# Performance work log

Measured on AMD Instinct MI355X. Metric: run time of the kernel, lower is better.

## Reference

```python
import jax, jax.numpy as jnp
import numpy as np

D_EMB = 1024
D_ATTN = 1024
NUM_HEADS = 16
HEAD_DIM = D_ATTN // NUM_HEADS
SEQ = 2048
BS = 2


def setup_inputs() -> dict:
    key = jax.random.key(0)
    ks = jax.random.split(key, 6)
    s = 1.0 / np.sqrt(D_EMB)
    return {
        "x": jax.random.normal(ks[0], (BS, SEQ, D_EMB), dtype=jnp.float32),
        "W_q": jax.random.uniform(ks[1], (D_ATTN, D_EMB), jnp.float32, -s, s),
        "W_k": jax.random.uniform(ks[2], (D_ATTN, D_EMB), jnp.float32, -s, s),
        "W_v": jax.random.uniform(ks[3], (D_ATTN, D_EMB), jnp.float32, -s, s),
        "W_o": jax.random.uniform(ks[4], (D_ATTN, D_ATTN), jnp.float32, -s, s),
        "b_o": jax.random.uniform(ks[5], (D_ATTN,), jnp.float32, -s, s),
    }


def reference(x, W_q, W_k, W_v, W_o, b_o):
    bs, seq_len, _ = x.shape
    # QKV projections (torch Linear: x @ W.T)
    q = jnp.einsum('bse,ae->bsa', x, W_q).reshape(bs, seq_len, NUM_HEADS, HEAD_DIM)
    k = jnp.einsum('bse,ae->bsa', x, W_k).reshape(bs, seq_len, NUM_HEADS, HEAD_DIM)
    v = jnp.einsum('bse,ae->bsa', x, W_v).reshape(bs, seq_len, NUM_HEADS, HEAD_DIM)
    # [b, h, s, d]
    q = q.transpose(0, 2, 1, 3)
    k = k.transpose(0, 2, 1, 3)
    v = v.transpose(0, 2, 1, 3)
    # scores [b, h, s, s] with causal mask
    scores = jnp.einsum('bhqd,bhkd->bhqk', q, k)
    causal = jnp.tril(jnp.ones((seq_len, seq_len), dtype=bool))
    scores = jnp.where(causal, scores, -jnp.inf)
    attn = jax.nn.softmax(scores / np.sqrt(HEAD_DIM), axis=-1)
    # dropout p=0.0 -> identity
    ctx = jnp.einsum('bhqk,bhkd->bhqd', attn, v)
    ctx = ctx.transpose(0, 2, 1, 3).reshape(bs, seq_len, D_ATTN)
    return jnp.einsum('bsa,oa->bso', ctx, W_o) + b_o
```

## Files before the change

kernel.cpp:

```cpp
#include <hip/hip_runtime.h>
#include <stdint.h>

#define SEQ   2048
#define DEMB  1024
#define NH    16
#define HD    64
#define MROWS 4096

typedef __bf16 bf16x8 __attribute__((ext_vector_type(8)));
typedef __bf16 bf16x4 __attribute__((ext_vector_type(4)));
typedef float  f32x4  __attribute__((ext_vector_type(4)));

#define MFMA(a, b, c) __builtin_amdgcn_mfma_f32_16x16x32_bf16((a), (b), (c), 0, 0, 0)

static __device__ __forceinline__ uint16_t f2bf(float f) {
  union { __bf16 b; uint16_t u; } c;
  c.b = (__bf16)f;
  return c.u;
}

static __device__ __forceinline__ ushort4 pack4(f32x4 f) {
  union { bf16x4 b; ushort4 u; } c;
  c.b[0] = (__bf16)f[0]; c.b[1] = (__bf16)f[1];
  c.b[2] = (__bf16)f[2]; c.b[3] = (__bf16)f[3];
  return c.u;
}

static __device__ __forceinline__ bf16x8 ldb8(const uint16_t* p) {
  union { uint4 i; bf16x8 b; } u;
  u.i = *(const uint4*)p;
  return u.b;
}

static __device__ __forceinline__ void gld_lds16(const uint16_t* g, uint16_t* l) {
  __builtin_amdgcn_global_load_lds(
      (const __attribute__((address_space(1))) uint32_t*)(g),
      (__attribute__((address_space(3))) uint32_t*)(l),
      16, 0, 0);
}

__global__ __launch_bounds__(256) void cvt_all(const float* __restrict__ x,
                                               const float* __restrict__ wq,
                                               const float* __restrict__ wk,
                                               const float* __restrict__ wv,
                                               const float* __restrict__ wo,
                                               uint16_t* __restrict__ xb,
                                               uint16_t* __restrict__ wqkv,
                                               uint16_t* __restrict__ wob) {
  const int bid = blockIdx.x;
  const float* src; uint16_t* dst; int off;
  if (bid < 4096)      { src = x;  dst = xb;                 off = bid; }
  else if (bid < 5120) { src = wq; dst = wqkv;               off = bid - 4096; }
  else if (bid < 6144) { src = wk; dst = wqkv + (1u << 20);  off = bid - 5120; }
  else if (bid < 7168) { src = wv; dst = wqkv + (2u << 20);  off = bid - 6144; }
  else                 { src = wo; dst = wob;                off = bid - 7168; }
  const int i = (off * 256 + threadIdx.x) * 4;
  float4 v = *(const float4*)(src + i);
  f32x4 f; f[0] = v.x; f[1] = v.y; f[2] = v.z; f[3] = v.w;
  *(ushort4*)(dst + i) = pack4(f);
}

__global__ __launch_bounds__(512, 2) void gemm_qkv(const uint16_t* __restrict__ A,
                                                   const uint16_t* __restrict__ B,
                                                   uint16_t* __restrict__ Cq,
                                                   uint16_t* __restrict__ Ck,
                                                   uint16_t* __restrict__ Cvt) {
  constexpr int K = 1024;
  __shared__ uint16_t lds[57344];

  const int bcol = blockIdx.x * 192;
  const int brow = blockIdx.y << 8;

  const int t  = threadIdx.x;
  const int l  = t & 63;
  const int li = l & 15, lg = l >> 4;
  const int w  = t >> 6;
  const int wm = w >> 2;
  const int wn = w & 3;

  const int srow = t >> 3;
  const int scol = ((t & 7) ^ (srow & 7)) << 3;
  const uint16_t* gA = A + (size_t)(brow + srow) * K + scol;
  const uint16_t* gB = B + (size_t)(bcol + srow) * K + scol;

  auto stage = [&](int buf, int k0) {
    uint16_t* as = lds + buf * 16384;
    uint16_t* bs = lds + 32768 + buf * 12288;
    gld_lds16(gA + k0,                    as + t * 8);
    gld_lds16(gA + (size_t)64 * K + k0,   as + 4096 + t * 8);
    gld_lds16(gA + (size_t)128 * K + k0,  as + 8192 + t * 8);
    gld_lds16(gA + (size_t)192 * K + k0,  as + 12288 + t * 8);
    gld_lds16(gB + k0,                    bs + t * 8);
    gld_lds16(gB + (size_t)64 * K + k0,   bs + 4096 + t * 8);
    gld_lds16(gB + (size_t)128 * K + k0,  bs + 8192 + t * 8);
  };

  const int sw = li & 7;
  auto ldA = [&](int buf, int kh, int fi) {
    const int row = wm * 128 + fi * 16 + li;
    return ldb8(&lds[buf * 16384 + (row << 6) + ((((kh << 2) + lg) ^ sw) << 3)]);
  };
  auto ldB = [&](int buf, int kh, int ni) {
    const int row = wn * 48 + ni * 16 + li;
    return ldb8(&lds[32768 + buf * 12288 + (row << 6) + ((((kh << 2) + lg) ^ sw) << 3)]);
  };

  f32x4 acc[8][3] = {};

  stage(0, 0);
  __syncthreads();
  int cur = 0;

  for (int k0 = 0; k0 < K; k0 += 64) {
    if (k0 + 64 < K) stage(cur ^ 1, k0 + 64);

#pragma unroll
    for (int kh = 0; kh < 2; ++kh) {
      bf16x8 af[8], bfr[3];
#pragma unroll
      for (int ni = 0; ni < 3; ++ni) bfr[ni] = ldB(cur, kh, ni);
#pragma unroll
      for (int fi = 0; fi < 8; ++fi) af[fi] = ldA(cur, kh, fi);
      __builtin_amdgcn_s_setprio(1);
#pragma unroll
      for (int fi = 0; fi < 8; ++fi)
#pragma unroll
        for (int ni = 0; ni < 3; ++ni)
          acc[fi][ni] = MFMA(af[fi], bfr[ni], acc[fi][ni]);
      __builtin_amdgcn_s_setprio(0);
    }

    __syncthreads();
    cur ^= 1;
  }

  uint16_t* slab = lds + w * 6800;
  bool anyV = false;

#pragma unroll
  for (int mi = 0; mi < 8; ++mi) {
#pragma unroll
    for (int ni = 0; ni < 3; ++ni) {
      const int col = bcol + wn * 48 + ni * 16 + li;
      const int row = brow + wm * 128 + mi * 16 + lg * 4;
      if (col < 1024) {
#pragma unroll
        for (int r = 0; r < 4; ++r)
          Cq[(size_t)(row + r) * 1024 + col] = f2bf(acc[mi][ni][r] * 0.18033688f);
      } else if (col < 2048) {
#pragma unroll
        for (int r = 0; r < 4; ++r)
          Ck[(size_t)(row + r) * 1024 + (col - 1024)] = f2bf(acc[mi][ni][r]);
      } else {
        anyV = true;
        *(ushort4*)&slab[(ni * 16 + li) * 136 + mi * 16 + lg * 4] = pack4(acc[mi][ni]);
      }
    }
  }

  if (anyV) {
    asm volatile("s_waitcnt lgkmcnt(0)" ::: "memory");
    const int m0 = brow + wm * 128;
    const size_t mbase = (size_t)((m0 >> 11) << 10) * 2048 + (m0 & 2047);
#pragma unroll
    for (int cc = 0; cc < 12; ++cc) {
      const int c_loc = cc * 4 + lg;
      const int cglob = bcol + wn * 48 + c_loc;
      if (cglob >= 2048) {
        const int c = cglob - 2048;
        uint4 v = *(const uint4*)&slab[c_loc * 136 + li * 8];
        *(uint4*)(Cvt + (size_t)c * 2048 + mbase + li * 8) = v;
      }
    }
  }
}

__global__ __launch_bounds__(512, 2) void gemm_out(const uint16_t* __restrict__ A,
                                                   const uint16_t* __restrict__ B,
                                                   float* __restrict__ Cf,
                                                   const float* __restrict__ bias) {
  constexpr int K = 1024;
  __shared__ uint16_t As[2][128 * 64];
  __shared__ uint16_t Bs[2][128 * 64];

  const int bcol = blockIdx.x << 7;
  const int brow = blockIdx.y << 7;

  const int t  = threadIdx.x;
  const int l  = t & 63;
  const int li = l & 15, lg = l >> 4;
  const int w  = t >> 6;
  const int wm = w >> 2;
  const int wn = w & 3;

  const int srow = t >> 3;
  const int scol = ((t & 7) ^ (srow & 7)) << 3;
  const uint16_t* gA = A + (size_t)(brow + srow) * K + scol;
  const uint16_t* gB = B + (size_t)(bcol + srow) * K + scol;

  auto stage = [&](int buf, int k0) {
    gld_lds16(gA + k0,                  &As[buf][t * 8]);
    gld_lds16(gA + (size_t)64 * K + k0, &As[buf][4096 + t * 8]);
    gld_lds16(gB + k0,                  &Bs[buf][t * 8]);
    gld_lds16(gB + (size_t)64 * K + k0, &Bs[buf][4096 + t * 8]);
  };

  const int sw = li & 7;
  auto ldA = [&](int buf, int kh, int fi) {
    const int row = wm * 64 + fi * 16 + li;
    return ldb8(&As[buf][(row << 6) + ((((kh << 2) + lg) ^ sw) << 3)]);
  };
  auto ldB = [&](int buf, int kh, int ni) {
    const int row = wn * 32 + ni * 16 + li;
    return ldb8(&Bs[buf][(row << 6) + ((((kh << 2) + lg) ^ sw) << 3)]);
  };

  f32x4 acc[4][2] = {};

  stage(0, 0);
  __syncthreads();
  int cur = 0;

  for (int k0 = 0; k0 < K; k0 += 64) {
    if (k0 + 64 < K) stage(cur ^ 1, k0 + 64);

#pragma unroll
    for (int kh = 0; kh < 2; ++kh) {
      bf16x8 af[4], bfr[2];
#pragma unroll
      for (int ni = 0; ni < 2; ++ni) bfr[ni] = ldB(cur, kh, ni);
#pragma unroll
      for (int fi = 0; fi < 4; ++fi) af[fi] = ldA(cur, kh, fi);
      __builtin_amdgcn_s_setprio(1);
#pragma unroll
      for (int fi = 0; fi < 4; ++fi)
#pragma unroll
        for (int ni = 0; ni < 2; ++ni)
          acc[fi][ni] = MFMA(af[fi], bfr[ni], acc[fi][ni]);
      __builtin_amdgcn_s_setprio(0);
    }

    __syncthreads();
    cur ^= 1;
  }

#pragma unroll
  for (int mi = 0; mi < 4; ++mi) {
#pragma unroll
    for (int ni = 0; ni < 2; ++ni) {
      const int row = brow + wm * 64 + mi * 16 + lg * 4;
      const int col = bcol + wn * 32 + ni * 16 + li;
      const float bv = bias[col];
#pragma unroll
      for (int r = 0; r < 4; ++r)
        Cf[(size_t)(row + r) * 1024 + col] = acc[mi][ni][r] + bv;
    }
  }
}

__global__ __launch_bounds__(256, 3) void attn_fwd(const uint16_t* __restrict__ Q,
                                                   const uint16_t* __restrict__ K,
                                                   const uint16_t* __restrict__ Vt,
                                                   uint16_t* __restrict__ ctx) {
  const int id   = blockIdx.x;
  const int rank = id >> 3;
  const int bh   = (id & 7) * 4 + (rank >> 4);
  const int pr   = rank & 15;
  const int b = bh >> 4, h = bh & 15;

  const int t  = threadIdx.x;
  const int w  = t >> 6, l = t & 63;
  const int li = l & 15, lg = l >> 4;

  __shared__ uint16_t Kl[2][64 * 64];
  __shared__ uint16_t Vl[2][64 * 64];
  __shared__ uint16_t P[4][16][72];

  const uint16_t* Kg = K + (size_t)(b * 2048) * 1024 + h * 64;
  const uint16_t* Vg = Vt + (size_t)(b * 1024 + h * 64) * 2048;

  const int srow = t >> 3;
  const int scol = ((t & 7) * 8) ^ ((srow & 7) * 8);

  auto stage = [&](int buf, int kt2) {
    const int kb2 = kt2 << 6;
    gld_lds16(Kg + (size_t)(kb2 + srow) * 1024 + scol,      &Kl[buf][t * 8]);
    gld_lds16(Kg + (size_t)(kb2 + 32 + srow) * 1024 + scol, &Kl[buf][2048 + t * 8]);
    gld_lds16(Vg + (size_t)srow * 2048 + kb2 + scol,        &Vl[buf][t * 8]);
    gld_lds16(Vg + (size_t)(32 + srow) * 2048 + kb2 + scol, &Vl[buf][2048 + t * 8]);
  };

  const int fsw = (li & 7) * 8;
  int cur = 0;

#pragma unroll 1
  for (int ph = 0; ph < 2; ++ph) {
    const int qbl  = ph ? (31 - pr) : pr;
    const int qrow = (qbl << 6) + (w << 4);
    const uint16_t* qp = Q + (size_t)(b * 2048 + qrow + li) * 1024 + h * 64 + lg * 8;
    const bf16x8 q0 = ldb8(qp);
    const bf16x8 q1 = ldb8(qp + 32);

    f32x4 o[4] = {};
    float l_r = 0.f;

    stage(cur, 0);
    __syncthreads();

    for (int kt = 0; kt <= qbl; ++kt) {
      if (kt < qbl) stage(cur ^ 1, kt + 1);

      const uint16_t* Kc = &Kl[cur][0];
      const uint16_t* Vc = &Vl[cur][0];

      f32x4 s[4];
      __builtin_amdgcn_s_setprio(1);
#pragma unroll
      for (int tt = 0; tt < 4; ++tt) {
        const uint16_t* kr = Kc + (tt * 16 + li) * 64;
        f32x4 z = {};
        z = MFMA(ldb8(kr + ((lg * 8) ^ fsw)), q0, z);
        z = MFMA(ldb8(kr + ((32 + lg * 8) ^ fsw)), q1, z);
        s[tt] = z;
      }
      __builtin_amdgcn_s_setprio(0);

      bf16x8 vf[4][2];
#pragma unroll
      for (int dt = 0; dt < 4; ++dt) {
        const uint16_t* vr = Vc + (dt * 16 + li) * 64;
        vf[dt][0] = ldb8(vr + ((lg * 8) ^ fsw));
        vf[dt][1] = ldb8(vr + ((32 + lg * 8) ^ fsw));
      }

      if (kt == qbl) {
        const int qloc = (w << 4) + li;
#pragma unroll
        for (int tt = 0; tt < 4; ++tt) {
          const int key = (tt << 4) + (lg << 2);
#pragma unroll
          for (int r = 0; r < 4; ++r)
            if (key + r > qloc) s[tt][r] = -1e30f;
        }
      }

      float lsum = 0.f;
      ushort4 pk[4];
#pragma unroll
      for (int tt = 0; tt < 4; ++tt) {
        f32x4 p;
        p[0] = __builtin_amdgcn_exp2f(s[tt][0]);
        p[1] = __builtin_amdgcn_exp2f(s[tt][1]);
        p[2] = __builtin_amdgcn_exp2f(s[tt][2]);
        p[3] = __builtin_amdgcn_exp2f(s[tt][3]);
        lsum += (p[0] + p[1]) + (p[2] + p[3]);
        pk[tt] = pack4(p);
      }
      l_r += lsum;

#pragma unroll
      for (int tt = 0; tt < 4; ++tt)
        *(ushort4*)&P[w][li][(tt << 4) + (lg << 2)] = pk[tt];
      asm volatile("s_waitcnt lgkmcnt(0)" ::: "memory");

      const bf16x8 pb0 = ldb8(&P[w][li][lg * 8]);
      const bf16x8 pb1 = ldb8(&P[w][li][32 + lg * 8]);
      __builtin_amdgcn_s_setprio(1);
#pragma unroll
      for (int dt = 0; dt < 4; ++dt) {
        o[dt] = MFMA(vf[dt][0], pb0, o[dt]);
        o[dt] = MFMA(vf[dt][1], pb1, o[dt]);
      }
      __builtin_amdgcn_s_setprio(0);

      __syncthreads();
      cur ^= 1;
    }

    l_r += __shfl_xor(l_r, 16);
    l_r += __shfl_xor(l_r, 32);
    const float inv = 1.0f / l_r;
    const int qg = b * 2048 + qrow + li;
#pragma unroll
    for (int dt = 0; dt < 4; ++dt) {
      f32x4 ov = o[dt];
      ov[0] *= inv; ov[1] *= inv; ov[2] *= inv; ov[3] *= inv;
      *(ushort4*)(ctx + (size_t)qg * 1024 + h * 64 + (dt << 4) + (lg << 2)) = pack4(ov);
    }
  }
}

extern "C" void kernel_launch(void* const* d_in, const int* in_sizes, int n_in,
                              void* d_out, int out_size, void* d_ws, size_t ws_size,
                              hipStream_t stream) {
  const float* x  = (const float*)d_in[0];
  const float* Wq = (const float*)d_in[1];
  const float* Wk = (const float*)d_in[2];
  const float* Wv = (const float*)d_in[3];
  const float* Wo = (const float*)d_in[4];
  const float* bo = (const float*)d_in[5];
  float* out = (float*)d_out;

  char* ws = (char*)d_ws;
  uint16_t* xb   = (uint16_t*)(ws);
  uint16_t* Wqkv = (uint16_t*)(ws + ( 8u << 20));
  uint16_t* Wob  = (uint16_t*)(ws + (14u << 20));
  uint16_t* Qb   = (uint16_t*)(ws + (16u << 20));
  uint16_t* Kb   = (uint16_t*)(ws + (24u << 20));
  uint16_t* Vt   = (uint16_t*)(ws + (32u << 20));
  uint16_t* Ctx  = (uint16_t*)(ws);

  cvt_all<<<8192, 256, 0, stream>>>(x, Wq, Wk, Wv, Wo, xb, Wqkv, Wob);

  gemm_qkv<<<dim3(16, 16), 512, 0, stream>>>(xb, Wqkv, Qb, Kb, Vt);

  attn_fwd<<<512, 256, 0, stream>>>(Qb, Kb, Vt, Ctx);

  gemm_out<<<dim3(8, 32), 512, 0, stream>>>(Ctx, Wob, out, bo);
}
```

Baseline: 99.12 us.

## Triple-buffer LDS prefetch with vmcnt-gated barriers in GEMMs and attention

Replaces double buffering with a deeper prefetch pipeline in all three hot kernels. The QKV GEMM keeps three A buffers and two B buffers, while the output GEMM and the attention kernel keep three buffers, loading two tiles ahead. Each iteration waits with explicit s_waitcnt vmcnt plus a raw barrier instead of __syncthreads, so later loads stay in flight while the current tile is computed. The aim is to hide global-to-LDS latency. The cost is much larger LDS use, which likely lowers blocks per CU for the GEMMs. The attention launch bound is also lowered from 3 to 2.

Measured after the change: 100.7 us. About the same (+1.6%).

```diff
diff --git a/kernel.cpp b/kernel.cpp
--- a/kernel.cpp
+++ b/kernel.cpp
@@ -12,6 +12,7 @@
 typedef float  f32x4  __attribute__((ext_vector_type(4)));
 
 #define MFMA(a, b, c) __builtin_amdgcn_mfma_f32_16x16x32_bf16((a), (b), (c), 0, 0, 0)
+#define VMCNT(n) asm volatile("s_waitcnt vmcnt(" #n ")" ::: "memory")
 
 static __device__ __forceinline__ uint16_t f2bf(float f) {
   union { __bf16 b; uint16_t u; } c;
@@ -66,7 +67,7 @@
                                                    uint16_t* __restrict__ Ck,
                                                    uint16_t* __restrict__ Cvt) {
   constexpr int K = 1024;
-  __shared__ uint16_t lds[57344];
+  __shared__ uint16_t lds[73728];
 
   const int bcol = blockIdx.x * 192;
   const int brow = blockIdx.y << 8;
@@ -83,13 +84,15 @@
   const uint16_t* gA = A + (size_t)(brow + srow) * K + scol;
   const uint16_t* gB = B + (size_t)(bcol + srow) * K + scol;
 
-  auto stage = [&](int buf, int k0) {
+  auto stageA = [&](int buf, int k0) {
     uint16_t* as = lds + buf * 16384;
-    uint16_t* bs = lds + 32768 + buf * 12288;
     gld_lds16(gA + k0,                    as + t * 8);
     gld_lds16(gA + (size_t)64 * K + k0,   as + 4096 + t * 8);
     gld_lds16(gA + (size_t)128 * K + k0,  as + 8192 + t * 8);
     gld_lds16(gA + (size_t)192 * K + k0,  as + 12288 + t * 8);
+  };
+  auto stageB = [&](int buf, int k0) {
+    uint16_t* bs = lds + 49152 + buf * 12288;
     gld_lds16(gB + k0,                    bs + t * 8);
     gld_lds16(gB + (size_t)64 * K + k0,   bs + 4096 + t * 8);
     gld_lds16(gB + (size_t)128 * K + k0,  bs + 8192 + t * 8);
@@ -102,25 +105,30 @@
   };
   auto ldB = [&](int buf, int kh, int ni) {
     const int row = wn * 48 + ni * 16 + li;
-    return ldb8(&lds[32768 + buf * 12288 + (row << 6) + ((((kh << 2) + lg) ^ sw) << 3)]);
+    return ldb8(&lds[49152 + buf * 12288 + (row << 6) + ((((kh << 2) + lg) ^ sw) << 3)]);
   };
 
   f32x4 acc[8][3] = {};
 
-  stage(0, 0);
-  __syncthreads();
-  int cur = 0;
-
-  for (int k0 = 0; k0 < K; k0 += 64) {
-    if (k0 + 64 < K) stage(cur ^ 1, k0 + 64);
-
+  stageB(0, 0);
+  stageA(0, 0);
+  stageA(1, 64);
+  VMCNT(4);
+  __builtin_amdgcn_s_barrier();
+
+  for (int kt = 0; kt < 16; ++kt) {
+    const int k0 = kt << 6;
+    if (kt + 1 < 16) stageB((kt + 1) & 1, k0 + 64);
+    if (kt + 2 < 16) stageA((kt + 2) % 3, k0 + 128);
+
+    const int ab = kt % 3, bb = kt & 1;
 #pragma unroll
     for (int kh = 0; kh < 2; ++kh) {
       bf16x8 af[8], bfr[3];
 #pragma unroll
-      for (int ni = 0; ni < 3; ++ni) bfr[ni] = ldB(cur, kh, ni);
-#pragma unroll
-      for (int fi = 0; fi < 8; ++fi) af[fi] = ldA(cur, kh, fi);
+      for (int ni = 0; ni < 3; ++ni) bfr[ni] = ldB(bb, kh, ni);
+#pragma unroll
+      for (int fi = 0; fi < 8; ++fi) af[fi] = ldA(ab, kh, fi);
       __builtin_amdgcn_s_setprio(1);
 #pragma unroll
       for (int fi = 0; fi < 8; ++fi)
@@ -130,9 +138,14 @@
       __builtin_amdgcn_s_setprio(0);
     }
 
-    __syncthreads();
-    cur ^= 1;
-  }
+    if (kt + 1 < 16) {
+      if (kt + 2 < 16) VMCNT(4);
+      else             VMCNT(0);
+      __builtin_amdgcn_s_barrier();
+    }
+  }
+
+  __syncthreads();
 
   uint16_t* slab = lds + w * 6800;
   bool anyV = false;
@@ -180,8 +193,7 @@
                                                    float* __restrict__ Cf,
                                                    const float* __restrict__ bias) {
   constexpr int K = 1024;
-  __shared__ uint16_t As[2][128 * 64];
-  __shared__ uint16_t Bs[2][128 * 64];
+  __shared__ uint16_t lds[49152];
 
   const int bcol = blockIdx.x << 7;
   const int brow = blockIdx.y << 7;
@@ -199,38 +211,43 @@
   const uint16_t* gB = B + (size_t)(bcol + srow) * K + scol;
 
   auto stage = [&](int buf, int k0) {
-    gld_lds16(gA + k0,                  &As[buf][t * 8]);
-    gld_lds16(gA + (size_t)64 * K + k0, &As[buf][4096 + t * 8]);
-    gld_lds16(gB + k0,                  &Bs[buf][t * 8]);
-    gld_lds16(gB + (size_t)64 * K + k0, &Bs[buf][4096 + t * 8]);
+    uint16_t* as = lds + buf * 8192;
+    uint16_t* bs = lds + 24576 + buf * 8192;
+    gld_lds16(gA + k0,                  as + t * 8);
+    gld_lds16(gA + (size_t)64 * K + k0, as + 4096 + t * 8);
+    gld_lds16(gB + k0,                  bs + t * 8);
+    gld_lds16(gB + (size_t)64 * K + k0, bs + 4096 + t * 8);
   };
 
   const int sw = li & 7;
   auto ldA = [&](int buf, int kh, int fi) {
     const int row = wm * 64 + fi * 16 + li;
-    return ldb8(&As[buf][(row << 6) + ((((kh << 2) + lg) ^ sw) << 3)]);
+    return ldb8(&lds[buf * 8192 + (row << 6) + ((((kh << 2) + lg) ^ sw) << 3)]);
   };
   auto ldB = [&](int buf, int kh, int ni) {
     const int row = wn * 32 + ni * 16 + li;
-    return ldb8(&Bs[buf][(row << 6) + ((((kh << 2) + lg) ^ sw) << 3)]);
+    return ldb8(&lds[24576 + buf * 8192 + (row << 6) + ((((kh << 2) + lg) ^ sw) << 3)]);
   };
 
   f32x4 acc[4][2] = {};
 
   stage(0, 0);
-  __syncthreads();
-  int cur = 0;
-
-  for (int k0 = 0; k0 < K; k0 += 64) {
-    if (k0 + 64 < K) stage(cur ^ 1, k0 + 64);
-
+  stage(1, 64);
+  VMCNT(4);
+  __builtin_amdgcn_s_barrier();
+
+  for (int kt = 0; kt < 16; ++kt) {
+    const int k0 = kt << 6;
+    if (kt + 2 < 16) stage((kt + 2) % 3, k0 + 128);
+
+    const int cb = kt % 3;
 #pragma unroll
     for (int kh = 0; kh < 2; ++kh) {
       bf16x8 af[4], bfr[2];
 #pragma unroll
-      for (int ni = 0; ni < 2; ++ni) bfr[ni] = ldB(cur, kh, ni);
-#pragma unroll
-      for (int fi = 0; fi < 4; ++fi) af[fi] = ldA(cur, kh, fi);
+      for (int ni = 0; ni < 2; ++ni) bfr[ni] = ldB(cb, kh, ni);
+#pragma unroll
+      for (int fi = 0; fi < 4; ++fi) af[fi] = ldA(cb, kh, fi);
       __builtin_amdgcn_s_setprio(1);
 #pragma unroll
       for (int fi = 0; fi < 4; ++fi)
@@ -240,8 +257,11 @@
       __builtin_amdgcn_s_setprio(0);
     }
 
-    __syncthreads();
-    cur ^= 1;
+    if (kt + 1 < 16) {
+      if (kt + 2 < 16) VMCNT(4);
+      else             VMCNT(0);
+      __builtin_amdgcn_s_barrier();
+    }
   }
 
 #pragma unroll
@@ -258,7 +278,7 @@
   }
 }
 
-__global__ __launch_bounds__(256, 3) void attn_fwd(const uint16_t* __restrict__ Q,
+__global__ __launch_bounds__(256, 2) void attn_fwd(const uint16_t* __restrict__ Q,
                                                    const uint16_t* __restrict__ K,
                                                    const uint16_t* __restrict__ Vt,
                                                    uint16_t* __restrict__ ctx) {
@@ -272,8 +292,8 @@
   const int w  = t >> 6, l = t & 63;
   const int li = l & 15, lg = l >> 4;
 
-  __shared__ uint16_t Kl[2][64 * 64];
-  __shared__ uint16_t Vl[2][64 * 64];
+  __shared__ uint16_t Kl[3][64 * 64];
+  __shared__ uint16_t Vl[3][64 * 64];
   __shared__ uint16_t P[4][16][72];
 
   const uint16_t* Kg = K + (size_t)(b * 2048) * 1024 + h * 64;
@@ -291,11 +311,11 @@
   };
 
   const int fsw = (li & 7) * 8;
-  int cur = 0;
 
 #pragma unroll 1
   for (int ph = 0; ph < 2; ++ph) {
     const int qbl  = ph ? (31 - pr) : pr;
+    const int nkt  = qbl + 1;
     const int qrow = (qbl << 6) + (w << 4);
     const uint16_t* qp = Q + (size_t)(b * 2048 + qrow + li) * 1024 + h * 64 + lg * 8;
     const bf16x8 q0 = ldb8(qp);
@@ -304,14 +324,16 @@
     f32x4 o[4] = {};
     float l_r = 0.f;
 
-    stage(cur, 0);
-    __syncthreads();
-
-    for (int kt = 0; kt <= qbl; ++kt) {
-      if (kt < qbl) stage(cur ^ 1, kt + 1);
-
-      const uint16_t* Kc = &Kl[cur][0];
-      const uint16_t* Vc = &Vl[cur][0];
+    stage(0, 0);
+    stage(1, 1);
+    VMCNT(4);
+    __builtin_amdgcn_s_barrier();
+
+    for (int kt = 0; kt < nkt; ++kt) {
+      if (kt + 2 < nkt) stage((kt + 2) % 3, kt + 2);
+
+      const uint16_t* Kc = &Kl[kt % 3][0];
+      const uint16_t* Vc = &Vl[kt % 3][0];
 
       f32x4 s[4];
       __builtin_amdgcn_s_setprio(1);
@@ -373,9 +395,14 @@
       }
       __builtin_amdgcn_s_setprio(0);
 
-      __syncthreads();
-      cur ^= 1;
-    }
+      if (kt + 1 < nkt) {
+        if (kt + 2 < nkt) VMCNT(4);
+        else              VMCNT(0);
+        __builtin_amdgcn_s_barrier();
+      }
+    }
+
+    __syncthreads();
 
     l_r += __shfl_xor(l_r, 16);
     l_r += __shfl_xor(l_r, 32);
```

## Widen attention key tile to 128 with split K/V waits and reuse K buffer for P

Applied to the files above, without the earlier changes.

The attention kernel now processes 128 keys per iteration instead of 64, halving loop trips and barriers per query block. K and V are staged into separate LDS regions with explicit vmcnt waits, so QK^T can start once K has landed while V is still loading. The P scratch is carved out of the current K buffer after a barrier, removing the separate P array. LDS use doubles and occupancy drops from 3 to 2 blocks per SM. The diagonal tile now does extra masked work because of the coarser tile granularity.

Result: no change. 97.67 us (median of 2 runs) (-1.5%).

```diff
diff --git a/kernel.cpp b/kernel.cpp
--- a/kernel.cpp
+++ b/kernel.cpp
@@ -12,6 +12,13 @@
 typedef float  f32x4  __attribute__((ext_vector_type(4)));
 
 #define MFMA(a, b, c) __builtin_amdgcn_mfma_f32_16x16x32_bf16((a), (b), (c), 0, 0, 0)
+#define VMCNT(n) asm volatile("s_waitcnt vmcnt(" #n ")" ::: "memory")
+
+static __device__ __forceinline__ void bar() {
+  asm volatile("" ::: "memory");
+  __builtin_amdgcn_s_barrier();
+  asm volatile("" ::: "memory");
+}
 
 static __device__ __forceinline__ uint16_t f2bf(float f) {
   union { __bf16 b; uint16_t u; } c;
@@ -258,7 +265,7 @@
   }
 }
 
-__global__ __launch_bounds__(256, 3) void attn_fwd(const uint16_t* __restrict__ Q,
+__global__ __launch_bounds__(256, 2) void attn_fwd(const uint16_t* __restrict__ Q,
                                                    const uint16_t* __restrict__ K,
                                                    const uint16_t* __restrict__ Vt,
                                                    uint16_t* __restrict__ ctx) {
@@ -272,108 +279,113 @@
   const int w  = t >> 6, l = t & 63;
   const int li = l & 15, lg = l >> 4;
 
-  __shared__ uint16_t Kl[2][64 * 64];
-  __shared__ uint16_t Vl[2][64 * 64];
-  __shared__ uint16_t P[4][16][72];
+  __shared__ uint16_t Kl[2][128 * 64];
+  __shared__ uint16_t Vl[2][64 * 128];
 
   const uint16_t* Kg = K + (size_t)(b * 2048) * 1024 + h * 64;
   const uint16_t* Vg = Vt + (size_t)(b * 1024 + h * 64) * 2048;
 
-  const int srow = t >> 3;
-  const int scol = ((t & 7) * 8) ^ ((srow & 7) * 8);
-
-  auto stage = [&](int buf, int kt2) {
-    const int kb2 = kt2 << 6;
-    gld_lds16(Kg + (size_t)(kb2 + srow) * 1024 + scol,      &Kl[buf][t * 8]);
-    gld_lds16(Kg + (size_t)(kb2 + 32 + srow) * 1024 + scol, &Kl[buf][2048 + t * 8]);
-    gld_lds16(Vg + (size_t)srow * 2048 + kb2 + scol,        &Vl[buf][t * 8]);
-    gld_lds16(Vg + (size_t)(32 + srow) * 2048 + kb2 + scol, &Vl[buf][2048 + t * 8]);
-  };
-
-  const int fsw = (li & 7) * 8;
-  int cur = 0;
+  const int krow  = t >> 3;
+  const int kscol = ((t & 7) ^ (krow & 7)) << 3;
+  const int vrow  = t >> 4;
+  const int vscol = ((t & 15) ^ vrow) << 3;
+
+  auto stageK = [&](int buf, int kb) {
+#pragma unroll
+    for (int c = 0; c < 4; ++c)
+      gld_lds16(Kg + (size_t)(kb + c * 32 + krow) * 1024 + kscol,
+                &Kl[buf][c * 2048 + t * 8]);
+  };
+  auto stageV = [&](int buf, int kb) {
+#pragma unroll
+    for (int c = 0; c < 4; ++c)
+      gld_lds16(Vg + (size_t)(c * 16 + vrow) * 2048 + kb + vscol,
+                &Vl[buf][c * 2048 + t * 8]);
+  };
+
+  const int fsw = li & 7;
 
 #pragma unroll 1
   for (int ph = 0; ph < 2; ++ph) {
-    const int qbl  = ph ? (31 - pr) : pr;
+    const int qbl = ph ? (31 - pr) : pr;
+    const int nkt = (qbl >> 1) + 1;
     const int qrow = (qbl << 6) + (w << 4);
+    const int qglob = qrow + li;
     const uint16_t* qp = Q + (size_t)(b * 2048 + qrow + li) * 1024 + h * 64 + lg * 8;
-    const bf16x8 q0 = ldb8(qp);
-    const bf16x8 q1 = ldb8(qp + 32);
+    const bf16x8 q0v = ldb8(qp);
+    const bf16x8 q1v = ldb8(qp + 32);
 
     f32x4 o[4] = {};
     float l_r = 0.f;
-
-    stage(cur, 0);
-    __syncthreads();
-
-    for (int kt = 0; kt <= qbl; ++kt) {
-      if (kt < qbl) stage(cur ^ 1, kt + 1);
-
-      const uint16_t* Kc = &Kl[cur][0];
-      const uint16_t* Vc = &Vl[cur][0];
-
-      f32x4 s[4];
+    int cur = 0;
+
+    stageK(0, 0);
+    stageV(0, 0);
+    VMCNT(4);
+    bar();
+
+    for (int kt = 0; kt < nkt; ++kt) {
+      const int kb = kt << 7;
+      const bool pf = (kt + 1 < nkt);
+      if (pf) { stageK(cur ^ 1, kb + 128); stageV(cur ^ 1, kb + 128); }
+
+      f32x4 s[8];
       __builtin_amdgcn_s_setprio(1);
 #pragma unroll
-      for (int tt = 0; tt < 4; ++tt) {
-        const uint16_t* kr = Kc + (tt * 16 + li) * 64;
+      for (int tt = 0; tt < 8; ++tt) {
+        const uint16_t* kr = &Kl[cur][(tt * 16 + li) << 6];
         f32x4 z = {};
-        z = MFMA(ldb8(kr + ((lg * 8) ^ fsw)), q0, z);
-        z = MFMA(ldb8(kr + ((32 + lg * 8) ^ fsw)), q1, z);
+        z = MFMA(ldb8(kr + ((lg ^ fsw) << 3)), q0v, z);
+        z = MFMA(ldb8(kr + (((4 + lg) ^ fsw) << 3)), q1v, z);
         s[tt] = z;
       }
       __builtin_amdgcn_s_setprio(0);
 
-      bf16x8 vf[4][2];
-#pragma unroll
-      for (int dt = 0; dt < 4; ++dt) {
-        const uint16_t* vr = Vc + (dt * 16 + li) * 64;
-        vf[dt][0] = ldb8(vr + ((lg * 8) ^ fsw));
-        vf[dt][1] = ldb8(vr + ((32 + lg * 8) ^ fsw));
-      }
-
-      if (kt == qbl) {
-        const int qloc = (w << 4) + li;
-#pragma unroll
-        for (int tt = 0; tt < 4; ++tt) {
-          const int key = (tt << 4) + (lg << 2);
+      if (kb + 127 > qrow) {
+#pragma unroll
+        for (int tt = 0; tt < 8; ++tt) {
+          const int key = kb + (tt << 4) + (lg << 2);
 #pragma unroll
           for (int r = 0; r < 4; ++r)
-            if (key + r > qloc) s[tt][r] = -1e30f;
+            if (key + r > qglob) s[tt][r] = -1e30f;
         }
       }
 
+      if (pf) VMCNT(8); else VMCNT(0);
+      bar();
+
+      uint16_t* Pb = &Kl[cur][(w << 11) + (li << 7)];
       float lsum = 0.f;
-      ushort4 pk[4];
-#pragma unroll
-      for (int tt = 0; tt < 4; ++tt) {
+#pragma unroll
+      for (int tt = 0; tt < 8; ++tt) {
         f32x4 p;
         p[0] = __builtin_amdgcn_exp2f(s[tt][0]);
         p[1] = __builtin_amdgcn_exp2f(s[tt][1]);
         p[2] = __builtin_amdgcn_exp2f(s[tt][2]);
         p[3] = __builtin_amdgcn_exp2f(s[tt][3]);
         lsum += (p[0] + p[1]) + (p[2] + p[3]);
-        pk[tt] = pack4(p);
+        *(ushort4*)(Pb + ((((tt << 1) + (lg >> 1)) ^ li) << 3) + ((lg & 1) << 2)) = pack4(p);
       }
       l_r += lsum;
-
-#pragma unroll
-      for (int tt = 0; tt < 4; ++tt)
-        *(ushort4*)&P[w][li][(tt << 4) + (lg << 2)] = pk[tt];
       asm volatile("s_waitcnt lgkmcnt(0)" ::: "memory");
 
-      const bf16x8 pb0 = ldb8(&P[w][li][lg * 8]);
-      const bf16x8 pb1 = ldb8(&P[w][li][32 + lg * 8]);
+      bf16x8 pb[4];
+#pragma unroll
+      for (int ks = 0; ks < 4; ++ks)
+        pb[ks] = ldb8(Pb + ((((ks << 2) + lg) ^ li) << 3));
+
       __builtin_amdgcn_s_setprio(1);
 #pragma unroll
       for (int dt = 0; dt < 4; ++dt) {
-        o[dt] = MFMA(vf[dt][0], pb0, o[dt]);
-        o[dt] = MFMA(vf[dt][1], pb1, o[dt]);
+        const uint16_t* vr = &Vl[cur][(dt * 16 + li) << 7];
+#pragma unroll
+        for (int ks = 0; ks < 4; ++ks)
+          o[dt] = MFMA(ldb8(vr + ((((ks << 2) + lg) ^ li) << 3)), pb[ks], o[dt]);
       }
       __builtin_amdgcn_s_setprio(0);
 
-      __syncthreads();
+      if (pf) VMCNT(4);
+      bar();
       cur ^= 1;
     }
 
```
